# Kernel tuning notes

Measured on AMD Instinct MI355X. Metric: run time of the kernel, lower is better.

## Reference

```python
import jax, jax.numpy as jnp
import numpy as np
import math

NQ = 8          # qubits
DIM = 2 ** NQ   # 256-dim state vector
NVL = 4         # variational layers
EPS = 1e-5      # LayerNorm eps (torch default)


def _ln(x, g, b):
    m = jnp.mean(x, -1, keepdims=True)
    v = jnp.mean((x - m) ** 2, -1, keepdims=True)
    return (x - m) / jnp.sqrt(v + EPS) * g + b


def _apply_ry(state, q, theta):
    # state: (B, 256); qubit q is the 2**q 'pre' axis (PennyLane wire 0 = MSB)
    pre, post = 2 ** q, 2 ** (NQ - 1 - q)
    s = state.reshape(-1, pre, 2, post)
    c = jnp.cos(theta * 0.5)
    sn = jnp.sin(theta * 0.5)
    if jnp.ndim(theta) == 1:  # per-sample angle (input encoding)
        c = c[:, None, None]
        sn = sn[:, None, None]
    a0 = s[:, :, 0, :]
    a1 = s[:, :, 1, :]
    return jnp.stack([c * a0 - sn * a1, sn * a0 + c * a1], axis=2).reshape(state.shape)


def _apply_cnot(state, ctrl):
    # CNOT with control=ctrl, target=ctrl+1 (adjacent wires)
    pre = 2 ** ctrl
    s = state.reshape(-1, pre, 2, 2, 2 ** (NQ - 2 - ctrl))
    new = jnp.stack([s[:, :, 0], s[:, :, 1, ::-1]], axis=2)
    return new.reshape(state.shape)


def _vqc(inputs, weights):
    # inputs: (B, 8), weights: (4, 8) -> (B, 8) PauliZ expectations
    B = inputs.shape[0]
    # Hadamard layer on |0...0> -> uniform real superposition, amp = 1/16
    state = jnp.full((B, DIM), 1.0 / 16.0, dtype=inputs.dtype)
    for q in range(NQ):
        state = _apply_ry(state, q, inputs[:, q])
    for l in range(NVL):
        for c in range(0, NQ - 1, 2):
            state = _apply_cnot(state, c)
        for c in range(1, NQ - 1, 2):
            state = _apply_cnot(state, c)
        for q in range(NQ):
            state = _apply_ry(state, q, weights[l, q])
    p = state * state  # state stays real (H, RY, CNOT are real gates)
    zs = []
    for q in range(NQ):
        pr = p.reshape(B, 2 ** q, 2, 2 ** (NQ - 1 - q))
        zs.append(pr[:, :, 0, :].sum((1, 2)) - pr[:, :, 1, :].sum((1, 2)))
    return jnp.stack(zs, axis=1)


def reference(x, pe, emb_w, emb_b, emb_g, emb_bt, ip_w, ip_b, in_g, in_b,
              wq_i, wq_f, wq_g, wq_o, pi_w, pi_b, pf_w, pf_b, pg_w, pg_b,
              po_w, po_b, on_g, on_b, out_w, out_b):
    B, T, _ = x.shape
    H = emb_w.shape[0]
    # embedding + LayerNorm (dropout = identity in eval) + positional encoding
    emb = _ln(x @ emb_w.T + emb_b, emb_g, emb_bt) + pe[None, :T]

    def step(carry, x_t):
        h, c = carry
        comb = jnp.concatenate([x_t, h], axis=1)
        proj = _ln(jnp.tanh(comb @ ip_w.T + ip_b), in_g, in_b)
        i_t = jax.nn.sigmoid(_vqc(proj, wq_i) @ pi_w.T + pi_b)
        f_t = jax.nn.sigmoid(_vqc(proj, wq_f) @ pf_w.T + pf_b)
        g_t = jnp.tanh(_vqc(proj, wq_g) @ pg_w.T + pg_b)
        o_t = jax.nn.sigmoid(_vqc(proj, wq_o) @ po_w.T + po_b)
        c_n = f_t * c + i_t * g_t
        h_n = o_t * jnp.tanh(c_n)
        out_t = _ln(h_n + x_t, on_g, on_b)
        return (h_n, c_n), out_t

    h0 = jnp.zeros((B, H), x.dtype)
    xs = jnp.swapaxes(emb, 0, 1)  # (T, B, H)
    _, outs = jax.lax.scan(jax.checkpoint(step), (h0, h0), xs)
    out = jnp.swapaxes(outs, 0, 1)  # (B, T, H)
    return out @ out_w.T + out_b


def setup_inputs() -> dict:
    B, T, IN, H, OUT = 1024, 128, 8, 128, 1
    key = jax.random.key(0)
    ks = jax.random.split(key, 12)

    def kaiming_u(k, shape, fan_in):
        bnd = math.sqrt(6.0 / fan_in)
        return jax.random.uniform(k, shape, jnp.float32, -bnd, bnd)

    # sinusoidal positional encoding
    pe = np.zeros((T, H), np.float32)
    pos = np.arange(T, dtype=np.float32)[:, None]
    div = np.exp(np.arange(0, H, 2, dtype=np.float32) * (-math.log(10000.0) / H))
    pe[:, 0::2] = np.sin(pos * div)
    pe[:, 1::2] = np.cos(pos * div)

    return {
        'x': jax.random.normal(ks[0], (B, T, IN), jnp.float32),
        'pe': jnp.asarray(pe),
        'emb_w': kaiming_u(ks[1], (H, IN), IN), 'emb_b': jnp.zeros((H,), jnp.float32),
        'emb_g': jnp.ones((H,), jnp.float32), 'emb_bt': jnp.zeros((H,), jnp.float32),
        'ip_w': kaiming_u(ks[2], (NQ, 2 * H), 2 * H), 'ip_b': jnp.zeros((NQ,), jnp.float32),
        'in_g': jnp.ones((NQ,), jnp.float32), 'in_b': jnp.zeros((NQ,), jnp.float32),
        'wq_i': 0.01 * jax.random.normal(ks[3], (NVL, NQ), jnp.float32),
        'wq_f': 0.01 * jax.random.normal(ks[4], (NVL, NQ), jnp.float32),
        'wq_g': 0.01 * jax.random.normal(ks[5], (NVL, NQ), jnp.float32),
        'wq_o': 0.01 * jax.random.normal(ks[6], (NVL, NQ), jnp.float32),
        'pi_w': kaiming_u(ks[7], (H, NQ), NQ), 'pi_b': jnp.zeros((H,), jnp.float32),
        'pf_w': kaiming_u(ks[8], (H, NQ), NQ), 'pf_b': jnp.zeros((H,), jnp.float32),
        'pg_w': kaiming_u(ks[9], (H, NQ), NQ), 'pg_b': jnp.zeros((H,), jnp.float32),
        'po_w': kaiming_u(ks[10], (H, NQ), NQ), 'po_b': jnp.zeros((H,), jnp.float32),
        'on_g': jnp.ones((H,), jnp.float32), 'on_b': jnp.zeros((H,), jnp.float32),
        'out_w': kaiming_u(ks[11], (OUT, H), H), 'out_b': jnp.zeros((OUT,), jnp.float32),
    }
```

## Files before the change

kernel.cpp:

```cpp
#include <hip/hip_runtime.h>

#define Tv 128

typedef float v2 __attribute__((ext_vector_type(2)));

__device__ __forceinline__ v2 pkfma(v2 a, v2 b, v2 c) {
  return __builtin_elementwise_fma(a, b, c);
}

template<int CTRL>
__device__ __forceinline__ float dppx(float x) {
  return __int_as_float(__builtin_amdgcn_update_dpp(0, __float_as_int(x), CTRL, 0xF, 0xF, true));
}
__device__ __forceinline__ float dpp_rm(float x, int ctrl, int rm) {
  switch (ctrl) {
    default: return 0.f;
    case 0x111: return __int_as_float(__builtin_amdgcn_update_dpp(0, __float_as_int(x), 0x111, 0xF, 0xF, true));
    case 0x112: return __int_as_float(__builtin_amdgcn_update_dpp(0, __float_as_int(x), 0x112, 0xF, 0xF, true));
    case 0x114: return __int_as_float(__builtin_amdgcn_update_dpp(0, __float_as_int(x), 0x114, 0xF, 0xF, true));
    case 0x118: return __int_as_float(__builtin_amdgcn_update_dpp(0, __float_as_int(x), 0x118, 0xF, 0xF, true));
    case 0x142: return __int_as_float(__builtin_amdgcn_update_dpp(0, __float_as_int(x), 0x142, 0xA, 0xF, true));
    case 0x143: return __int_as_float(__builtin_amdgcn_update_dpp(0, __float_as_int(x), 0x143, 0xC, 0xF, true));
  }
}
__device__ __forceinline__ float wave_sum(float x) {
  x += dpp_rm(x, 0x111, 0xF);
  x += dpp_rm(x, 0x112, 0xF);
  x += dpp_rm(x, 0x114, 0xF);
  x += dpp_rm(x, 0x118, 0xF);
  x += dpp_rm(x, 0x142, 0xA);
  x += dpp_rm(x, 0x143, 0xC);
  return __int_as_float(__builtin_amdgcn_readlane(__float_as_int(x), 63));
}
template<int M>
__device__ __forceinline__ float lane_xor(float x) {
  if constexpr (M == 1)       return dppx<0xB1>(x);
  else if constexpr (M == 2)  return dppx<0x4E>(x);
  else if constexpr (M == 8)  return dppx<0x128>(x);
  else if constexpr (M == 32) return __shfl_xor(x, 32, 64);
  else return __int_as_float(__builtin_amdgcn_ds_swizzle(__float_as_int(x), (M << 10) | 0x1F));
}
__device__ __forceinline__ float bperm(int addr, float x) {
  return __int_as_float(__builtin_amdgcn_ds_bpermute(addr, __float_as_int(x)));
}
__device__ __forceinline__ float rdlane(float x, int l) {
  return __int_as_float(__builtin_amdgcn_readlane(__float_as_int(x), l));
}
__device__ __forceinline__ float fast_rcp(float x){ return __builtin_amdgcn_rcpf(x); }
__device__ __forceinline__ float fast_rsq(float x){ return __builtin_amdgcn_rsqf(x); }
__device__ __forceinline__ float tanh_(float x){
  float e = __expf(2.0f * x);
  return 1.0f - 2.0f * fast_rcp(e + 1.0f);
}
__device__ __forceinline__ float sigm_(float x){
  return fast_rcp(1.0f + __expf(-x));
}

__device__ __forceinline__ float transpose_reduce8(const v2* P2, int L) {
  const int bb0 = L & 1, bb1 = L & 2, bb2 = L & 4;
  float q_[4];
  #pragma unroll
  for (int k = 0; k < 4; k++) {
    float keep = bb0 ? P2[k].y : P2[k].x;
    float send = bb0 ? P2[k].x : P2[k].y;
    q_[k] = keep + lane_xor<1>(send);
  }
  float r_[2];
  #pragma unroll
  for (int k = 0; k < 2; k++) {
    float keep = bb1 ? q_[2 * k + 1] : q_[2 * k];
    float send = bb1 ? q_[2 * k]     : q_[2 * k + 1];
    r_[k] = keep + lane_xor<2>(send);
  }
  float u;
  {
    float keep = bb2 ? r_[1] : r_[0];
    float send = bb2 ? r_[0] : r_[1];
    u = keep + lane_xor<4>(send);
  }
  u += lane_xor<8>(u); u += lane_xor<16>(u); u += lane_xor<32>(u);
  return u;
}

template<int M>
__device__ __forceinline__ void ry_lane_t(v2* S, float ts) {
  v2 ts2 = {ts, ts};
  #pragma unroll
  for (int k = 0; k < 4; k++) {
    v2 o;
    o.x = lane_xor<M>(S[k].x);
    o.y = lane_xor<M>(S[k].y);
    S[k] = pkfma(ts2, o, S[k]);
  }
}


struct __align__(16) SMem {
  float tt[4][36];
  float ipb[8][4];
  float zbuf[32];
  float embp[2][2];
  float projp[2][8];
  float outp[2][4];
};

__global__ __launch_bounds__(128, 2) void qlstm_kernel(
    const float* __restrict__ x,     const float* __restrict__ pe,
    const float* __restrict__ emb_w, const float* __restrict__ emb_b,
    const float* __restrict__ emb_g, const float* __restrict__ emb_bt,
    const float* __restrict__ ip_w,  const float* __restrict__ ip_b,
    const float* __restrict__ in_g,  const float* __restrict__ in_b,
    const float* __restrict__ wq_i,  const float* __restrict__ wq_f,
    const float* __restrict__ wq_gt, const float* __restrict__ wq_o,
    const float* __restrict__ pi_w,  const float* __restrict__ pi_b,
    const float* __restrict__ pf_w,  const float* __restrict__ pf_b,
    const float* __restrict__ pg_w,  const float* __restrict__ pg_b,
    const float* __restrict__ po_w,  const float* __restrict__ po_b,
    const float* __restrict__ on_g,  const float* __restrict__ on_b,
    const float* __restrict__ out_w, const float* __restrict__ out_b,
    float* __restrict__ out)
{
  __shared__ SMem sm;
  const int tid = threadIdx.x;
  const int b   = blockIdx.x;
  const int w   = tid >> 6;
  const int L   = tid & 63;
  const int l5  = L & 31;
  const int gate = w * 2 + (L >> 5);
  const int o8  = L & 7;

  {
    int gg = tid >> 5, rem = tid & 31;
    const float* wsel = (gg == 0) ? wq_i : (gg == 1) ? wq_f : (gg == 2) ? wq_gt : wq_o;
    float th = wsel[rem] * 0.5f;
    float cc = __cosf(th), ss = __sinf(th);
    sm.tt[gg][rem] = ss * fast_rcp(cc);
    float v = cc;
    v *= lane_xor<1>(v); v *= lane_xor<2>(v); v *= lane_xor<4>(v);
    v *= lane_xor<8>(v); v *= lane_xor<16>(v);
    if (rem == 0) sm.tt[gg][32] = v * v;
  }
  if (tid < 8) {
    sm.ipb[tid][0] = ip_b[tid];
    sm.ipb[tid][1] = in_g[tid];
    sm.ipb[tid][2] = in_b[tid];
    sm.ipb[tid][3] = 0.0f;
  }

  const int j = tid;
  v2 EW[4];
  {
    float4 a = *reinterpret_cast<const float4*>(emb_w + j * 8);
    float4 c = *reinterpret_cast<const float4*>(emb_w + j * 8 + 4);
    EW[0] = {a.x, a.y}; EW[1] = {a.z, a.w}; EW[2] = {c.x, c.y}; EW[3] = {c.z, c.w};
  }
  float ebb = emb_b[j], egg = emb_g[j], ebt = emb_bt[j];
  v2 IPW1[4], IPW2[4];
  #pragma unroll
  for (int k = 0; k < 4; k++) {
    IPW1[k] = {ip_w[(2 * k) * 256 + j],       ip_w[(2 * k + 1) * 256 + j]};
    IPW2[k] = {ip_w[(2 * k) * 256 + 128 + j], ip_w[(2 * k + 1) * 256 + 128 + j]};
  }
  v2 GW[4][4];
  #pragma unroll
  for (int gg = 0; gg < 4; gg++) {
    const float* pw = (gg == 0) ? pi_w : (gg == 1) ? pf_w : (gg == 2) ? pg_w : po_w;
    float4 a = *reinterpret_cast<const float4*>(pw + j * 8);
    float4 c = *reinterpret_cast<const float4*>(pw + j * 8 + 4);
    GW[gg][0] = {a.x, a.y}; GW[gg][1] = {a.z, a.w};
    GW[gg][2] = {c.x, c.y}; GW[gg][3] = {c.z, c.w};
  }
  float gb[4] = {pi_b[j], pf_b[j], pg_b[j], po_b[j]};
  float ong = on_g[j], onb = on_b[j], ow_ = out_w[j];
  float outb = out_b[0];
  float a_ = ong * ow_;

  const int grp = L & 32;
  int aC0, aC1;
  {
    int l1 = l5 ^ ((l5 & 16) >> 1) ^ ((l5 & 4) >> 1);
    int lb = l1 ^ ((l1 & 8) >> 1) ^ ((l1 & 2) >> 1);
    aC0 = (grp | lb) << 2;
    aC1 = (grp | (lb ^ 16)) << 2;
  }

  const int sg16 = (l5 & 16) << 27;
  const int sg8  = (l5 & 8)  << 28;
  const int sg4  = (l5 & 4)  << 29;
  const int sg2  = (l5 & 2)  << 30;
  const int sg1  = (l5 & 1)  << 31;

  float h = 0.f, c = 0.f;
  const float* xbase = x + (size_t)b * Tv * 8;

  {
    float uw = transpose_reduce8(EW, L);
    float eb1 = wave_sum(ebb);
    if (L < 8) sm.projp[w][L] = uw;
    if (L == 0) sm.embp[w][0] = eb1;
  }
  __syncthreads();

  v2 WB[4]; float bS;
  {
    #pragma unroll
    for (int k = 0; k < 4; k++) {
      WB[k].x = (sm.projp[0][2 * k]     + sm.projp[1][2 * k])     * 0.0078125f;
      WB[k].y = (sm.projp[0][2 * k + 1] + sm.projp[1][2 * k + 1]) * 0.0078125f;
    }
    bS = (sm.embp[0][0] + sm.embp[1][0]) * 0.0078125f;
  }
  float4 ipbv = *reinterpret_cast<float4*>(&sm.ipb[o8][0]);
  v2 LT0[4], LT1[4], LNTS[4];
  float LTS[4][5];
  float ct2g = sm.tt[gate][32];
  {
    const float* tg = sm.tt[gate];
    #pragma unroll
    for (int l = 0; l < 4; l++) {
      float4 qa = *reinterpret_cast<const float4*>(tg + l * 8);
      float4 qb = *reinterpret_cast<const float4*>(tg + l * 8 + 4);
      LT0[l]  = {qa.x, qa.x};
      LT1[l]  = {qa.y, qa.y};
      LNTS[l] = {-qa.z, qa.z};
      float tq[5] = {qa.w, qb.x, qb.y, qb.z, qb.w};
      #pragma unroll
      for (int q = 0; q < 5; q++) {
        int m = 16 >> q;
        LTS[l][q] = (l5 & m) ? tq[q] : -tq[q];
      }
    }
  }

  float e;
  {
    float4 a = *reinterpret_cast<const float4*>(xbase);
    float4 cq = *reinterpret_cast<const float4*>(xbase + 4);
    v2 XT[4] = {{a.x,a.y},{a.z,a.w},{cq.x,cq.y},{cq.z,cq.w}};
    v2 acc = XT[0] * EW[0];
    acc = pkfma(XT[1], EW[1], acc);
    acc = pkfma(XT[2], EW[2], acc);
    acc = pkfma(XT[3], EW[3], acc);
    float er = ebb + acc.x + acc.y;
    float s2 = wave_sum(er * er);
    float r0 = wave_sum(a_), r1 = wave_sum(onb * ow_);
    if (L == 0) {
      sm.embp[w][1] = s2;
      sm.outp[w][0] = r0; sm.outp[w][1] = r1;
    }
    __syncthreads();
    v2 mac = XT[0] * WB[0];
    mac = pkfma(XT[1], WB[1], mac);
    mac = pkfma(XT[2], WB[2], mac);
    mac = pkfma(XT[3], WB[3], mac);
    float mn = mac.x + mac.y + bS;
    float s2t = sm.embp[0][1] + sm.embp[1][1];
    float vr = fmaf(s2t, 0.0078125f, -mn * mn);
    float inv = fast_rsq(vr + 1e-5f);
    e = (er - mn) * inv * egg + ebt + pe[j];
  }
  const float SW = sm.outp[0][0] + sm.outp[1][0];
  const float KB = sm.outp[0][1] + sm.outp[1][1] + outb;

  #pragma unroll 1
  for (int t = 0; t < Tv; t++) {
    v2 XN[4]; float pen;
    {
      int tn = (t + 1) & (Tv - 1);
      float4 a = *reinterpret_cast<const float4*>(xbase + tn * 8);
      float4 cq = *reinterpret_cast<const float4*>(xbase + tn * 8 + 4);
      XN[0] = {a.x,a.y}; XN[1] = {a.z,a.w}; XN[2] = {cq.x,cq.y}; XN[3] = {cq.z,cq.w};
      pen = pe[tn * 128 + j];
    }

    const v2 e2 = {e, e}, h2 = {h, h};
    v2 P2[4];
    #pragma unroll
    for (int k = 0; k < 4; k++)
      P2[k] = pkfma(e2, IPW1[k], h2 * IPW2[k]);
    float u = transpose_reduce8(P2, L);
    if (L < 8) sm.projp[w][L] = u;
    __syncthreads();
    u += sm.projp[1 - w][o8];
    if (t && tid == 0) {
      float sy  = sm.outp[0][0] + sm.outp[1][0];
      float sy2 = sm.outp[0][1] + sm.outp[1][1];
      float sya = sm.outp[0][2] + sm.outp[1][2];
      float mn2 = sy * 0.0078125f;
      float vr2 = fmaf(sy2, 0.0078125f, -mn2 * mn2);
      float inv2 = fast_rsq(vr2 + 1e-5f);
      out[b * Tv + t - 1] = fmaf(inv2, sya - mn2 * SW, KB);
    }

    float tv = tanh_(u + ipbv.x);
    float m1 = tv, m2 = tv * tv;
    m1 += lane_xor<1>(m1); m2 += lane_xor<1>(m2);
    m1 += lane_xor<2>(m1); m2 += lane_xor<2>(m2);
    m1 += lane_xor<4>(m1); m2 += lane_xor<4>(m2);
    float pm = m1 * 0.125f;
    float pv = fmaf(m2, 0.125f, -pm * pm);
    float theta = (tv - pm) * fast_rsq(pv + 1e-5f) * ipbv.y + ipbv.z;
    float ph = theta * 0.5f;
    float cE = __cosf(ph), sE = __sinf(ph);
    float fm = cE - sE, fp = cE + sE;
    float f_[16];
    #pragma unroll
    for (int qq = 0; qq < 8; qq++) {
      f_[2 * qq]     = rdlane(fm, qq);
      f_[2 * qq + 1] = rdlane(fp, qq);
    }

    v2 S[4];
    {
      float g01_[4];
      #pragma unroll
      for (int i = 0; i < 4; i++)
        g01_[i] = f_[(i >> 1) & 1] * f_[2 + (i & 1)];
      float s3 = (l5 & 16) ? f_[7]  : f_[6];
      float s4 = (l5 & 8)  ? f_[9]  : f_[8];
      float s5 = (l5 & 4)  ? f_[11] : f_[10];
      float s6 = (l5 & 2)  ? f_[13] : f_[12];
      float s7 = (l5 & 1)  ? f_[15] : f_[14];
      float lf = s3 * s4 * s5 * s6 * s7 * 0.0625f;
      const v2 F45 = {f_[4], f_[5]};
      #pragma unroll
      for (int k = 0; k < 4; k++) {
        float tk = lf * g01_[k];
        v2 tk2 = {tk, tk};
        S[k] = tk2 * F45;
      }
    }

    #pragma unroll
    for (int l = 0; l < 4; l++) {
      v2 N0, N1, N2, N3;
      N0.x = bperm(aC0, S[0].x); N0.y = bperm(aC1, S[0].y);
      N1.x = bperm(aC1, S[1].y); N1.y = bperm(aC0, S[1].x);
      N2.x = bperm(aC0, S[3].x); N2.y = bperm(aC1, S[3].y);
      N3.x = bperm(aC1, S[2].y); N3.y = bperm(aC0, S[2].x);
      S[0] = N0; S[1] = N1; S[2] = N2; S[3] = N3;
      {
        v2 t0 = LT0[l];
        v2 a0 = S[0], a1 = S[1];
        S[0] = pkfma(-t0, S[2], S[0]);
        S[2] = pkfma( t0, a0,  S[2]);
        S[1] = pkfma(-t0, S[3], S[1]);
        S[3] = pkfma( t0, a1,  S[3]);
      }
      {
        v2 t1 = LT1[l];
        v2 a0 = S[0], a2 = S[2];
        S[0] = pkfma(-t1, S[1], S[0]);
        S[1] = pkfma( t1, a0,  S[1]);
        S[2] = pkfma(-t1, S[3], S[2]);
        S[3] = pkfma( t1, a2,  S[3]);
      }
      {
        v2 nts = LNTS[l];
        #pragma unroll
        for (int k = 0; k < 4; k++) {
          v2 aa = S[k];
          v2 sw = __builtin_shufflevector(aa, aa, 1, 0);
          S[k] = pkfma(nts, sw, aa);
        }
      }
      ry_lane_t<16>(S, LTS[l][0]);
      ry_lane_t<8>(S, LTS[l][1]);
      ry_lane_t<4>(S, LTS[l][2]);
      ry_lane_t<2>(S, LTS[l][3]);
      ry_lane_t<1>(S, LTS[l][4]);
    }

    {
      v2 P[4];
      #pragma unroll
      for (int k = 0; k < 4; k++) P[k] = S[k] * S[k];
      v2 A = P[0] + P[2];
      v2 B = P[1] + P[3];
      v2 D = (P[0] - P[2]) + (P[1] - P[3]);
      v2 Ev = A - B;
      v2 G = A + B;
      float z0p = D.x + D.y;
      float z1p = Ev.x + Ev.y;
      float z2p = G.x - G.y;
      float T = G.x + G.y;
      int Ti = __float_as_int(T);
      v2 ZP[4];
      ZP[0] = {z0p, z1p};
      ZP[1] = {z2p, __int_as_float(Ti ^ sg16)};
      ZP[2] = {__int_as_float(Ti ^ sg8), __int_as_float(Ti ^ sg4)};
      ZP[3] = {__int_as_float(Ti ^ sg2), __int_as_float(Ti ^ sg1)};
      const int cb0 = l5 & 1, cb1 = l5 & 2, cb2 = l5 & 4;
      float mq[4];
      #pragma unroll
      for (int k = 0; k < 4; k++) {
        float keep = cb0 ? ZP[k].y : ZP[k].x;
        float send = cb0 ? ZP[k].x : ZP[k].y;
        mq[k] = keep + lane_xor<1>(send);
      }
      float mr[2];
      #pragma unroll
      for (int k = 0; k < 2; k++) {
        float keep = cb1 ? mq[2 * k + 1] : mq[2 * k];
        float send = cb1 ? mq[2 * k]     : mq[2 * k + 1];
        mr[k] = keep + lane_xor<2>(send);
      }
      float zu;
      {
        float keep = cb2 ? mr[1] : mr[0];
        float send = cb2 ? mr[0] : mr[1];
        zu = keep + lane_xor<4>(send);
      }
      zu += lane_xor<8>(zu);
      zu += lane_xor<16>(zu);
      if (l5 < 8) sm.zbuf[gate * 8 + l5] = zu * ct2g;
    }

    v2 acc = XN[0] * EW[0];
    acc = pkfma(XN[1], EW[1], acc);
    acc = pkfma(XN[2], EW[2], acc);
    acc = pkfma(XN[3], EW[3], acc);
    float en_raw = ebb + acc.x + acc.y;
    {
      float s2n = wave_sum(en_raw * en_raw);
      if (L == 0) sm.embp[w][0] = s2n;
    }
    __syncthreads();

    float acg[4];
    #pragma unroll
    for (int gg = 0; gg < 4; gg++) {
      float4 za0 = *reinterpret_cast<float4*>(&sm.zbuf[gg * 8]);
      float4 za1 = *reinterpret_cast<float4*>(&sm.zbuf[gg * 8 + 4]);
      v2 Z0 = {za0.x, za0.y}, Z1 = {za0.z, za0.w};
      v2 Z2 = {za1.x, za1.y}, Z3 = {za1.z, za1.w};
      v2 av = Z0 * GW[gg][0];
      av = pkfma(Z1, GW[gg][1], av);
      av = pkfma(Z2, GW[gg][2], av);
      av = pkfma(Z3, GW[gg][3], av);
      acg[gg] = gb[gg] + av.x + av.y;
    }
    float it = sigm_(acg[0]), ft = sigm_(acg[1]), gt = tanh_(acg[2]), ot = sigm_(acg[3]);
    c = ft * c + it * gt;
    h = ot * tanh_(c);

    float en;
    {
      float s2 = sm.embp[0][0] + sm.embp[1][0];
      v2 mac = XN[0] * WB[0];
      mac = pkfma(XN[1], WB[1], mac);
      mac = pkfma(XN[2], WB[2], mac);
      mac = pkfma(XN[3], WB[3], mac);
      float mn = mac.x + mac.y + bS;
      float vr = fmaf(s2, 0.0078125f, -mn * mn);
      float inv = fast_rsq(vr + 1e-5f);
      en = (en_raw - mn) * inv * egg + ebt + pen;
    }

    {
      float y = h + e;
      float ry0 = wave_sum(y), ry1 = wave_sum(y * y), ry2 = wave_sum(y * a_);
      if (L == 0) { sm.outp[w][0] = ry0; sm.outp[w][1] = ry1; sm.outp[w][2] = ry2; }
    }
    e = en;
  }

  __syncthreads();
  if (tid == 0) {
    float sy  = sm.outp[0][0] + sm.outp[1][0];
    float sy2 = sm.outp[0][1] + sm.outp[1][1];
    float sya = sm.outp[0][2] + sm.outp[1][2];
    float mn2 = sy * 0.0078125f;
    float vr2 = fmaf(sy2, 0.0078125f, -mn2 * mn2);
    float inv2 = fast_rsq(vr2 + 1e-5f);
    out[b * Tv + Tv - 1] = fmaf(inv2, sya - mn2 * SW, KB);
  }
}

extern "C" void kernel_launch(void* const* d_in, const int* in_sizes, int n_in,
                              void* d_out, int out_size, void* d_ws, size_t ws_size,
                              hipStream_t stream) {
  qlstm_kernel<<<dim3(1024), dim3(128), 0, stream>>>(
      (const float*)d_in[0],  (const float*)d_in[1],  (const float*)d_in[2],  (const float*)d_in[3],
      (const float*)d_in[4],  (const float*)d_in[5],  (const float*)d_in[6],  (const float*)d_in[7],
      (const float*)d_in[8],  (const float*)d_in[9],  (const float*)d_in[10], (const float*)d_in[11],
      (const float*)d_in[12], (const float*)d_in[13], (const float*)d_in[14], (const float*)d_in[15],
      (const float*)d_in[16], (const float*)d_in[17], (const float*)d_in[18], (const float*)d_in[19],
      (const float*)d_in[20], (const float*)d_in[21], (const float*)d_in[22], (const float*)d_in[23],
      (const float*)d_in[24], (const float*)d_in[25],
      (float*)d_out);
}
```

Before: 476.8 us.

## Make each wave own all 128 hidden units to drop a per-step barrier

Every lane now handles two hidden units (j and j+64), so both waves hold the full hidden state redundantly. The cross-wave shared-memory exchanges for the input projection, embedding LayerNorm and output LayerNorm go away, leaving one __syncthreads per timestep on a double-buffered zbuf. Each lane does roughly twice the ALU work for the projection, gate and LSTM updates, and the per-layer RY tangents are reloaded from LDS inside the loop instead of being held in registers. The output is written in the same step it is computed rather than one step later.

Result: slower. 497.3 us (+4.3%).

```diff
diff --git a/kernel.cpp b/kernel.cpp
--- a/kernel.cpp
+++ b/kernel.cpp
@@ -4,6 +4,7 @@
 
 typedef float v2 __attribute__((ext_vector_type(2)));
 
+__device__ __forceinline__ v2 mkv2(float a, float b) { v2 r; r.x = a; r.y = b; return r; }
 __device__ __forceinline__ v2 pkfma(v2 a, v2 b, v2 c) {
   return __builtin_elementwise_fma(a, b, c);
 }
@@ -52,8 +53,11 @@
   float e = __expf(2.0f * x);
   return 1.0f - 2.0f * fast_rcp(e + 1.0f);
 }
-__device__ __forceinline__ float sigm_(float x){
-  return fast_rcp(1.0f + __expf(-x));
+__device__ __forceinline__ v2 sigm2(v2 x){
+  return mkv2(fast_rcp(1.0f + __expf(-x.x)), fast_rcp(1.0f + __expf(-x.y)));
+}
+__device__ __forceinline__ v2 tanh2(v2 x){
+  return mkv2(tanh_(x.x), tanh_(x.y));
 }
 
 __device__ __forceinline__ float transpose_reduce8(const v2* P2, int L) {
@@ -84,7 +88,7 @@
 
 template<int M>
 __device__ __forceinline__ void ry_lane_t(v2* S, float ts) {
-  v2 ts2 = {ts, ts};
+  v2 ts2 = mkv2(ts, ts);
   #pragma unroll
   for (int k = 0; k < 4; k++) {
     v2 o;
@@ -98,10 +102,7 @@
 struct __align__(16) SMem {
   float tt[4][36];
   float ipb[8][4];
-  float zbuf[32];
-  float embp[2][2];
-  float projp[2][8];
-  float outp[2][4];
+  float zbuf[2][32];
 };
 
 __global__ __launch_bounds__(128, 2) void qlstm_kernel(
@@ -128,6 +129,7 @@
   const int l5  = L & 31;
   const int gate = w * 2 + (L >> 5);
   const int o8  = L & 7;
+  const int jA  = L, jB = L + 64;
 
   {
     int gg = tid >> 5, rem = tid & 31;
@@ -147,33 +149,48 @@
     sm.ipb[tid][3] = 0.0f;
   }
 
-  const int j = tid;
-  v2 EW[4];
-  {
-    float4 a = *reinterpret_cast<const float4*>(emb_w + j * 8);
-    float4 c = *reinterpret_cast<const float4*>(emb_w + j * 8 + 4);
-    EW[0] = {a.x, a.y}; EW[1] = {a.z, a.w}; EW[2] = {c.x, c.y}; EW[3] = {c.z, c.w};
-  }
-  float ebb = emb_b[j], egg = emb_g[j], ebt = emb_bt[j];
-  v2 IPW1[4], IPW2[4];
+  v2 EW2[8];
+  {
+    float4 a0 = *reinterpret_cast<const float4*>(emb_w + jA * 8);
+    float4 a1 = *reinterpret_cast<const float4*>(emb_w + jA * 8 + 4);
+    float4 b0 = *reinterpret_cast<const float4*>(emb_w + jB * 8);
+    float4 b1 = *reinterpret_cast<const float4*>(emb_w + jB * 8 + 4);
+    EW2[0] = mkv2(a0.x, b0.x); EW2[1] = mkv2(a0.y, b0.y);
+    EW2[2] = mkv2(a0.z, b0.z); EW2[3] = mkv2(a0.w, b0.w);
+    EW2[4] = mkv2(a1.x, b1.x); EW2[5] = mkv2(a1.y, b1.y);
+    EW2[6] = mkv2(a1.z, b1.z); EW2[7] = mkv2(a1.w, b1.w);
+  }
+  v2 ebb2 = mkv2(emb_b[jA], emb_b[jB]);
+  v2 egg2 = mkv2(emb_g[jA], emb_g[jB]);
+  v2 ebt2 = mkv2(emb_bt[jA], emb_bt[jB]);
+  v2 IPW1A[4], IPW2A[4], IPW1B[4], IPW2B[4];
   #pragma unroll
   for (int k = 0; k < 4; k++) {
-    IPW1[k] = {ip_w[(2 * k) * 256 + j],       ip_w[(2 * k + 1) * 256 + j]};
-    IPW2[k] = {ip_w[(2 * k) * 256 + 128 + j], ip_w[(2 * k + 1) * 256 + 128 + j]};
-  }
-  v2 GW[4][4];
+    IPW1A[k] = mkv2(ip_w[(2 * k) * 256 + jA],       ip_w[(2 * k + 1) * 256 + jA]);
+    IPW2A[k] = mkv2(ip_w[(2 * k) * 256 + 128 + jA], ip_w[(2 * k + 1) * 256 + 128 + jA]);
+    IPW1B[k] = mkv2(ip_w[(2 * k) * 256 + jB],       ip_w[(2 * k + 1) * 256 + jB]);
+    IPW2B[k] = mkv2(ip_w[(2 * k) * 256 + 128 + jB], ip_w[(2 * k + 1) * 256 + 128 + jB]);
+  }
+  v2 GW2[4][8];
   #pragma unroll
   for (int gg = 0; gg < 4; gg++) {
     const float* pw = (gg == 0) ? pi_w : (gg == 1) ? pf_w : (gg == 2) ? pg_w : po_w;
-    float4 a = *reinterpret_cast<const float4*>(pw + j * 8);
-    float4 c = *reinterpret_cast<const float4*>(pw + j * 8 + 4);
-    GW[gg][0] = {a.x, a.y}; GW[gg][1] = {a.z, a.w};
-    GW[gg][2] = {c.x, c.y}; GW[gg][3] = {c.z, c.w};
-  }
-  float gb[4] = {pi_b[j], pf_b[j], pg_b[j], po_b[j]};
-  float ong = on_g[j], onb = on_b[j], ow_ = out_w[j];
+    float4 a0 = *reinterpret_cast<const float4*>(pw + jA * 8);
+    float4 a1 = *reinterpret_cast<const float4*>(pw + jA * 8 + 4);
+    float4 b0 = *reinterpret_cast<const float4*>(pw + jB * 8);
+    float4 b1 = *reinterpret_cast<const float4*>(pw + jB * 8 + 4);
+    GW2[gg][0] = mkv2(a0.x, b0.x); GW2[gg][1] = mkv2(a0.y, b0.y);
+    GW2[gg][2] = mkv2(a0.z, b0.z); GW2[gg][3] = mkv2(a0.w, b0.w);
+    GW2[gg][4] = mkv2(a1.x, b1.x); GW2[gg][5] = mkv2(a1.y, b1.y);
+    GW2[gg][6] = mkv2(a1.z, b1.z); GW2[gg][7] = mkv2(a1.w, b1.w);
+  }
+  v2 gb2[4] = {mkv2(pi_b[jA], pi_b[jB]), mkv2(pf_b[jA], pf_b[jB]),
+               mkv2(pg_b[jA], pg_b[jB]), mkv2(po_b[jA], po_b[jB])};
+  v2 ong2 = mkv2(on_g[jA], on_g[jB]);
+  v2 onb2 = mkv2(on_b[jA], on_b[jB]);
+  v2 ow2  = mkv2(out_w[jA], out_w[jB]);
   float outb = out_b[0];
-  float a_ = ong * ow_;
+  v2 a2 = ong2 * ow2;
 
   const int grp = L & 32;
   int aC0, aC1;
@@ -189,108 +206,85 @@
   const int sg4  = (l5 & 4)  << 29;
   const int sg2  = (l5 & 2)  << 30;
   const int sg1  = (l5 & 1)  << 31;
-
-  float h = 0.f, c = 0.f;
+  const int sR16 = (~l5 & 16) << 27;
+  const int sR8  = (~l5 & 8)  << 28;
+  const int sR4  = (~l5 & 4)  << 29;
+  const int sR2  = (~l5 & 2)  << 30;
+  const int sR1  = (~l5 & 1)  << 31;
+
+  v2 h2r = mkv2(0.f, 0.f), c2r = mkv2(0.f, 0.f);
   const float* xbase = x + (size_t)b * Tv * 8;
 
-  {
-    float uw = transpose_reduce8(EW, L);
-    float eb1 = wave_sum(ebb);
-    if (L < 8) sm.projp[w][L] = uw;
-    if (L == 0) sm.embp[w][0] = eb1;
-  }
   __syncthreads();
 
+  const float4 ipbv = *reinterpret_cast<float4*>(&sm.ipb[o8][0]);
+  const float ct2g = sm.tt[gate][32];
+  const float* tg = sm.tt[gate];
+
   v2 WB[4]; float bS;
   {
+    v2 C8[4];
+    #pragma unroll
+    for (int k = 0; k < 4; k++)
+      C8[k] = mkv2(EW2[2 * k].x + EW2[2 * k].y, EW2[2 * k + 1].x + EW2[2 * k + 1].y);
+    float uw = transpose_reduce8(C8, L);
+    float cs_[8];
+    #pragma unroll
+    for (int q = 0; q < 8; q++) cs_[q] = rdlane(uw, q) * 0.0078125f;
+    WB[0] = mkv2(cs_[0], cs_[1]); WB[1] = mkv2(cs_[2], cs_[3]);
+    WB[2] = mkv2(cs_[4], cs_[5]); WB[3] = mkv2(cs_[6], cs_[7]);
+    bS = wave_sum(ebb2.x + ebb2.y) * 0.0078125f;
+  }
+  const float SW = wave_sum(a2.x + a2.y);
+  const float KB = wave_sum(onb2.x * ow2.x + onb2.y * ow2.y) + outb;
+
+  v2 e2r;
+  {
+    float4 q0 = *reinterpret_cast<const float4*>(xbase);
+    float4 q1 = *reinterpret_cast<const float4*>(xbase + 4);
+    v2 XTv[4] = {mkv2(q0.x, q0.y), mkv2(q0.z, q0.w), mkv2(q1.x, q1.y), mkv2(q1.z, q1.w)};
+    v2 er2 = ebb2;
     #pragma unroll
     for (int k = 0; k < 4; k++) {
-      WB[k].x = (sm.projp[0][2 * k]     + sm.projp[1][2 * k])     * 0.0078125f;
-      WB[k].y = (sm.projp[0][2 * k + 1] + sm.projp[1][2 * k + 1]) * 0.0078125f;
-    }
-    bS = (sm.embp[0][0] + sm.embp[1][0]) * 0.0078125f;
-  }
-  float4 ipbv = *reinterpret_cast<float4*>(&sm.ipb[o8][0]);
-  v2 LT0[4], LT1[4], LNTS[4];
-  float LTS[4][5];
-  float ct2g = sm.tt[gate][32];
-  {
-    const float* tg = sm.tt[gate];
-    #pragma unroll
-    for (int l = 0; l < 4; l++) {
-      float4 qa = *reinterpret_cast<const float4*>(tg + l * 8);
-      float4 qb = *reinterpret_cast<const float4*>(tg + l * 8 + 4);
-      LT0[l]  = {qa.x, qa.x};
-      LT1[l]  = {qa.y, qa.y};
-      LNTS[l] = {-qa.z, qa.z};
-      float tq[5] = {qa.w, qb.x, qb.y, qb.z, qb.w};
-      #pragma unroll
-      for (int q = 0; q < 5; q++) {
-        int m = 16 >> q;
-        LTS[l][q] = (l5 & m) ? tq[q] : -tq[q];
-      }
-    }
-  }
-
-  float e;
-  {
-    float4 a = *reinterpret_cast<const float4*>(xbase);
-    float4 cq = *reinterpret_cast<const float4*>(xbase + 4);
-    v2 XT[4] = {{a.x,a.y},{a.z,a.w},{cq.x,cq.y},{cq.z,cq.w}};
-    v2 acc = XT[0] * EW[0];
-    acc = pkfma(XT[1], EW[1], acc);
-    acc = pkfma(XT[2], EW[2], acc);
-    acc = pkfma(XT[3], EW[3], acc);
-    float er = ebb + acc.x + acc.y;
-    float s2 = wave_sum(er * er);
-    float r0 = wave_sum(a_), r1 = wave_sum(onb * ow_);
-    if (L == 0) {
-      sm.embp[w][1] = s2;
-      sm.outp[w][0] = r0; sm.outp[w][1] = r1;
-    }
-    __syncthreads();
-    v2 mac = XT[0] * WB[0];
-    mac = pkfma(XT[1], WB[1], mac);
-    mac = pkfma(XT[2], WB[2], mac);
-    mac = pkfma(XT[3], WB[3], mac);
-    float mn = mac.x + mac.y + bS;
-    float s2t = sm.embp[0][1] + sm.embp[1][1];
-    float vr = fmaf(s2t, 0.0078125f, -mn * mn);
+      er2 = pkfma(mkv2(XTv[k].x, XTv[k].x), EW2[2 * k], er2);
+      er2 = pkfma(mkv2(XTv[k].y, XTv[k].y), EW2[2 * k + 1], er2);
+    }
+    float s2 = wave_sum(er2.x * er2.x + er2.y * er2.y);
+    v2 macc = XTv[0] * WB[0];
+    macc = pkfma(XTv[1], WB[1], macc);
+    macc = pkfma(XTv[2], WB[2], macc);
+    macc = pkfma(XTv[3], WB[3], macc);
+    float mn = macc.x + macc.y + bS;
+    float vr = fmaf(s2, 0.0078125f, -mn * mn);
     float inv = fast_rsq(vr + 1e-5f);
-    e = (er - mn) * inv * egg + ebt + pe[j];
-  }
-  const float SW = sm.outp[0][0] + sm.outp[1][0];
-  const float KB = sm.outp[0][1] + sm.outp[1][1] + outb;
+    v2 pe0 = mkv2(pe[jA], pe[jB]);
+    e2r = pkfma((er2 - mkv2(mn, mn)) * mkv2(inv, inv), egg2, ebt2) + pe0;
+  }
 
   #pragma unroll 1
   for (int t = 0; t < Tv; t++) {
-    v2 XN[4]; float pen;
+    v2 XNv[4]; v2 pen2;
     {
       int tn = (t + 1) & (Tv - 1);
-      float4 a = *reinterpret_cast<const float4*>(xbase + tn * 8);
-      float4 cq = *reinterpret_cast<const float4*>(xbase + tn * 8 + 4);
-      XN[0] = {a.x,a.y}; XN[1] = {a.z,a.w}; XN[2] = {cq.x,cq.y}; XN[3] = {cq.z,cq.w};
-      pen = pe[tn * 128 + j];
-    }
-
-    const v2 e2 = {e, e}, h2 = {h, h};
-    v2 P2[4];
-    #pragma unroll
-    for (int k = 0; k < 4; k++)
-      P2[k] = pkfma(e2, IPW1[k], h2 * IPW2[k]);
-    float u = transpose_reduce8(P2, L);
-    if (L < 8) sm.projp[w][L] = u;
-    __syncthreads();
-    u += sm.projp[1 - w][o8];
-    if (t && tid == 0) {
-      float sy  = sm.outp[0][0] + sm.outp[1][0];
-      float sy2 = sm.outp[0][1] + sm.outp[1][1];
-      float sya = sm.outp[0][2] + sm.outp[1][2];
-      float mn2 = sy * 0.0078125f;
-      float vr2 = fmaf(sy2, 0.0078125f, -mn2 * mn2);
-      float inv2 = fast_rsq(vr2 + 1e-5f);
-      out[b * Tv + t - 1] = fmaf(inv2, sya - mn2 * SW, KB);
-    }
+      float4 q0 = *reinterpret_cast<const float4*>(xbase + tn * 8);
+      float4 q1 = *reinterpret_cast<const float4*>(xbase + tn * 8 + 4);
+      XNv[0] = mkv2(q0.x, q0.y); XNv[1] = mkv2(q0.z, q0.w);
+      XNv[2] = mkv2(q1.x, q1.y); XNv[3] = mkv2(q1.z, q1.w);
+      pen2 = mkv2(pe[tn * 128 + jA], pe[tn * 128 + jB]);
+    }
+
+    const v2 eAs = mkv2(e2r.x, e2r.x), eBs = mkv2(e2r.y, e2r.y);
+    const v2 hAs = mkv2(h2r.x, h2r.x), hBs = mkv2(h2r.y, h2r.y);
+    v2 V[4];
+    #pragma unroll
+    for (int k = 0; k < 4; k++) {
+      v2 acc = hBs * IPW2B[k];
+      acc = pkfma(eBs, IPW1B[k], acc);
+      acc = pkfma(hAs, IPW2A[k], acc);
+      acc = pkfma(eAs, IPW1A[k], acc);
+      V[k] = acc;
+    }
+    float u = transpose_reduce8(V, L);
 
     float tv = tanh_(u + ipbv.x);
     float m1 = tv, m2 = tv * tv;
@@ -322,17 +316,18 @@
       float s6 = (l5 & 2)  ? f_[13] : f_[12];
       float s7 = (l5 & 1)  ? f_[15] : f_[14];
       float lf = s3 * s4 * s5 * s6 * s7 * 0.0625f;
-      const v2 F45 = {f_[4], f_[5]};
+      const v2 F45 = mkv2(f_[4], f_[5]);
       #pragma unroll
       for (int k = 0; k < 4; k++) {
         float tk = lf * g01_[k];
-        v2 tk2 = {tk, tk};
-        S[k] = tk2 * F45;
+        S[k] = mkv2(tk, tk) * F45;
       }
     }
 
     #pragma unroll
     for (int l = 0; l < 4; l++) {
+      float4 qa = *reinterpret_cast<const float4*>(tg + l * 8);
+      float4 qb = *reinterpret_cast<const float4*>(tg + l * 8 + 4);
       v2 N0, N1, N2, N3;
       N0.x = bperm(aC0, S[0].x); N0.y = bperm(aC1, S[0].y);
       N1.x = bperm(aC1, S[1].y); N1.y = bperm(aC0, S[1].x);
@@ -340,7 +335,7 @@
       N3.x = bperm(aC1, S[2].y); N3.y = bperm(aC0, S[2].x);
       S[0] = N0; S[1] = N1; S[2] = N2; S[3] = N3;
       {
-        v2 t0 = LT0[l];
+        v2 t0 = mkv2(qa.x, qa.x);
         v2 a0 = S[0], a1 = S[1];
         S[0] = pkfma(-t0, S[2], S[0]);
         S[2] = pkfma( t0, a0,  S[2]);
@@ -348,7 +343,7 @@
         S[3] = pkfma( t0, a1,  S[3]);
       }
       {
-        v2 t1 = LT1[l];
+        v2 t1 = mkv2(qa.y, qa.y);
         v2 a0 = S[0], a2 = S[2];
         S[0] = pkfma(-t1, S[1], S[0]);
         S[1] = pkfma( t1, a0,  S[1]);
@@ -356,7 +351,7 @@
         S[3] = pkfma( t1, a2,  S[3]);
       }
       {
-        v2 nts = LNTS[l];
+        v2 nts = mkv2(-qa.z, qa.z);
         #pragma unroll
         for (int k = 0; k < 4; k++) {
           v2 aa = S[k];
@@ -364,11 +359,11 @@
           S[k] = pkfma(nts, sw, aa);
         }
       }
-      ry_lane_t<16>(S, LTS[l][0]);
-      ry_lane_t<8>(S, LTS[l][1]);
-      ry_lane_t<4>(S, LTS[l][2]);
-      ry_lane_t<2>(S, LTS[l][3]);
-      ry_lane_t<1>(S, LTS[l][4]);
+      ry_lane_t<16>(S, __int_as_float(__float_as_int(qa.w) ^ sR16));
+      ry_lane_t<8> (S, __int_as_float(__float_as_int(qb.x) ^ sR8));
+      ry_lane_t<4> (S, __int_as_float(__float_as_int(qb.y) ^ sR4));
+      ry_lane_t<2> (S, __int_as_float(__float_as_int(qb.z) ^ sR2));
+      ry_lane_t<1> (S, __int_as_float(__float_as_int(qb.w) ^ sR1));
     }
 
     {
@@ -386,10 +381,10 @@
       float T = G.x + G.y;
       int Ti = __float_as_int(T);
       v2 ZP[4];
-      ZP[0] = {z0p, z1p};
-      ZP[1] = {z2p, __int_as_float(Ti ^ sg16)};
-      ZP[2] = {__int_as_float(Ti ^ sg8), __int_as_float(Ti ^ sg4)};
-      ZP[3] = {__int_as_float(Ti ^ sg2), __int_as_float(Ti ^ sg1)};
+      ZP[0] = mkv2(z0p, z1p);
+      ZP[1] = mkv2(z2p, __int_as_float(Ti ^ sg16));
+      ZP[2] = mkv2(__int_as_float(Ti ^ sg8), __int_as_float(Ti ^ sg4));
+      ZP[3] = mkv2(__int_as_float(Ti ^ sg2), __int_as_float(Ti ^ sg1));
       const int cb0 = l5 & 1, cb1 = l5 & 2, cb2 = l5 & 4;
       float mq[4];
       #pragma unroll
@@ -413,67 +408,66 @@
       }
       zu += lane_xor<8>(zu);
       zu += lane_xor<16>(zu);
-      if (l5 < 8) sm.zbuf[gate * 8 + l5] = zu * ct2g;
-    }
-
-    v2 acc = XN[0] * EW[0];
-    acc = pkfma(XN[1], EW[1], acc);
-    acc = pkfma(XN[2], EW[2], acc);
-    acc = pkfma(XN[3], EW[3], acc);
-    float en_raw = ebb + acc.x + acc.y;
+      if (l5 < 8) sm.zbuf[t & 1][gate * 8 + l5] = zu * ct2g;
+    }
+
+    v2 en_raw2 = ebb2;
+    #pragma unroll
+    for (int k = 0; k < 4; k++) {
+      en_raw2 = pkfma(mkv2(XNv[k].x, XNv[k].x), EW2[2 * k], en_raw2);
+      en_raw2 = pkfma(mkv2(XNv[k].y, XNv[k].y), EW2[2 * k + 1], en_raw2);
+    }
+    float s2n = wave_sum(en_raw2.x * en_raw2.x + en_raw2.y * en_raw2.y);
+
+    __syncthreads();
+
+    const float* zb = sm.zbuf[t & 1];
+    v2 acg2[4];
+    #pragma unroll
+    for (int gg = 0; gg < 4; gg++) {
+      float4 za0 = *reinterpret_cast<const float4*>(zb + gg * 8);
+      float4 za1 = *reinterpret_cast<const float4*>(zb + gg * 8 + 4);
+      v2 a = gb2[gg];
+      a = pkfma(mkv2(za0.x, za0.x), GW2[gg][0], a);
+      a = pkfma(mkv2(za0.y, za0.y), GW2[gg][1], a);
+      a = pkfma(mkv2(za0.z, za0.z), GW2[gg][2], a);
+      a = pkfma(mkv2(za0.w, za0.w), GW2[gg][3], a);
+      a = pkfma(mkv2(za1.x, za1.x), GW2[gg][4], a);
+      a = pkfma(mkv2(za1.y, za1.y), GW2[gg][5], a);
+      a = pkfma(mkv2(za1.z, za1.z), GW2[gg][6], a);
+      a = pkfma(mkv2(za1.w, za1.w), GW2[gg][7], a);
+      acg2[gg] = a;
+    }
+    v2 it2 = sigm2(acg2[0]), ft2 = sigm2(acg2[1]);
+    v2 gt2 = tanh2(acg2[2]), ot2 = sigm2(acg2[3]);
+    c2r = pkfma(ft2, c2r, it2 * gt2);
+    h2r = ot2 * tanh2(c2r);
+
+    v2 en2;
     {
-      float s2n = wave_sum(en_raw * en_raw);
-      if (L == 0) sm.embp[w][0] = s2n;
-    }
-    __syncthreads();
-
-    float acg[4];
-    #pragma unroll
-    for (int gg = 0; gg < 4; gg++) {
-      float4 za0 = *reinterpret_cast<float4*>(&sm.zbuf[gg * 8]);
-      float4 za1 = *reinterpret_cast<float4*>(&sm.zbuf[gg * 8 + 4]);
-      v2 Z0 = {za0.x, za0.y}, Z1 = {za0.z, za0.w};
-      v2 Z2 = {za1.x, za1.y}, Z3 = {za1.z, za1.w};
-      v2 av = Z0 * GW[gg][0];
-      av = pkfma(Z1, GW[gg][1], av);
-      av = pkfma(Z2, GW[gg][2], av);
-      av = pkfma(Z3, GW[gg][3], av);
-      acg[gg] = gb[gg] + av.x + av.y;
-    }
-    float it = sigm_(acg[0]), ft = sigm_(acg[1]), gt = tanh_(acg[2]), ot = sigm_(acg[3]);
-    c = ft * c + it * gt;
-    h = ot * tanh_(c);
-
-    float en;
+      v2 macc = XNv[0] * WB[0];
+      macc = pkfma(XNv[1], WB[1], macc);
+      macc = pkfma(XNv[2], WB[2], macc);
+      macc = pkfma(XNv[3], WB[3], macc);
+      float mn = macc.x + macc.y + bS;
+      float vr = fmaf(s2n, 0.0078125f, -mn * mn);
+      float inv = fast_rsq(vr + 1e-5f);
+      en2 = pkfma((en_raw2 - mkv2(mn, mn)) * mkv2(inv, inv), egg2, ebt2) + pen2;
+    }
+
     {
-      float s2 = sm.embp[0][0] + sm.embp[1][0];
-      v2 mac = XN[0] * WB[0];
-      mac = pkfma(XN[1], WB[1], mac);
-      mac = pkfma(XN[2], WB[2], mac);
-      mac = pkfma(XN[3], WB[3], mac);
-      float mn = mac.x + mac.y + bS;
-      float vr = fmaf(s2, 0.0078125f, -mn * mn);
-      float inv = fast_rsq(vr + 1e-5f);
-      en = (en_raw - mn) * inv * egg + ebt + pen;
-    }
-
-    {
-      float y = h + e;
-      float ry0 = wave_sum(y), ry1 = wave_sum(y * y), ry2 = wave_sum(y * a_);
-      if (L == 0) { sm.outp[w][0] = ry0; sm.outp[w][1] = ry1; sm.outp[w][2] = ry2; }
-    }
-    e = en;
-  }
-
-  __syncthreads();
-  if (tid == 0) {
-    float sy  = sm.outp[0][0] + sm.outp[1][0];
-    float sy2 = sm.outp[0][1] + sm.outp[1][1];
-    float sya = sm.outp[0][2] + sm.outp[1][2];
-    float mn2 = sy * 0.0078125f;
-    float vr2 = fmaf(sy2, 0.0078125f, -mn2 * mn2);
-    float inv2 = fast_rsq(vr2 + 1e-5f);
-    out[b * Tv + Tv - 1] = fmaf(inv2, sya - mn2 * SW, KB);
+      v2 y2 = h2r + e2r;
+      float sy  = wave_sum(y2.x + y2.y);
+      float syy = wave_sum(y2.x * y2.x + y2.y * y2.y);
+      float sya = wave_sum(y2.x * a2.x + y2.y * a2.y);
+      if (tid == 0) {
+        float mo = sy * 0.0078125f;
+        float vo = fmaf(syy, 0.0078125f, -mo * mo);
+        float io = fast_rsq(vo + 1e-5f);
+        out[b * Tv + t] = fmaf(io, sya - mo * SW, KB);
+      }
+    }
+    e2r = en2;
   }
 }
 
```
